# Kernel optimization log

Hardware: AMD Instinct MI355X
Metric: run time of the kernel (lower is better)

## Reference

```python
import jax, jax.numpy as jnp
import numpy as np

B, T, D, N = 32, 2048, 512, 512


def setup_inputs() -> dict:
    key = jax.random.key(0)
    ks = jax.random.split(key, 16)
    s_in = 1.0 / np.sqrt(D)
    s_h = 1.0 / np.sqrt(N)
    inp = {
        "x": jax.random.normal(ks[0], (B, T, D), dtype=jnp.float32),
        "W_i": jax.random.normal(ks[1], (D, N), dtype=jnp.float32) * s_in,
        "U_i": jax.random.normal(ks[2], (N, N), dtype=jnp.float32) * s_h,
        "W_f": jax.random.normal(ks[3], (D, N), dtype=jnp.float32) * s_in,
        "U_f": jax.random.normal(ks[4], (N, N), dtype=jnp.float32) * s_h,
        "W_g": jax.random.normal(ks[5], (D, N), dtype=jnp.float32) * s_in,
        "U_g": jax.random.normal(ks[6], (N, N), dtype=jnp.float32) * s_h,
        "W_c": jax.random.normal(ks[7], (D, N), dtype=jnp.float32) * s_in,
        "U_c": jax.random.normal(ks[8], (N, N), dtype=jnp.float32) * s_h,
        "W_o": jax.random.normal(ks[9], (N, N), dtype=jnp.float32) * s_h,
        "b_i": jnp.zeros((N,), dtype=jnp.float32),
        "b_f": jnp.zeros((N,), dtype=jnp.float32),
        "b_g": jnp.zeros((N,), dtype=jnp.float32),
        "b_c": jnp.zeros((N,), dtype=jnp.float32),
        "b_o": jnp.zeros((N,), dtype=jnp.float32),
    }
    return inp


def _lstm_forward(x, W_i, U_i, W_f, U_f, W_g, U_g, W_c, U_c, W_o,
                  b_i, b_f, b_g, b_c, b_o):
    # Precompute input-to-gate projections for all timesteps (same math,
    # hoisted out of the recurrence): [T, B, N] each
    xt = jnp.swapaxes(x, 0, 1)  # [T, B, N? no, D] -> [T, B, D]
    xi = jnp.einsum('tbd,dn->tbn', xt, W_i) + b_i
    xf = jnp.einsum('tbd,dn->tbn', xt, W_f) + b_f
    xg = jnp.einsum('tbd,dn->tbn', xt, W_g) + b_g
    xc = jnp.einsum('tbd,dn->tbn', xt, W_c) + b_c

    h0 = jnp.zeros((x.shape[0], U_i.shape[0]), dtype=x.dtype)
    c0 = jnp.zeros_like(h0)

    def step(carry, gates_t):
        h, c = carry
        xi_t, xf_t, xg_t, xc_t = gates_t
        i = jax.nn.sigmoid(xi_t + h @ U_i)
        f = jax.nn.sigmoid(xf_t + h @ U_f)
        g = jax.nn.sigmoid(xg_t + h @ U_g)  # original applies nonlin_i to g
        c_tilda = jnp.tanh(xc_t + h @ U_c)
        c_new = f * c + i * c_tilda
        h_new = g * jnp.tanh(c_new)
        return (h_new, c_new), h_new

    _, hs = jax.lax.scan(step, (h0, c0), (xi, xf, xg, xc))  # hs: [T, B, N]
    # output_fn: relu(h @ W_o + b_o), applied per timestep
    out = jax.nn.relu(jnp.einsum('tbn,nm->tbm', hs, W_o) + b_o)
    return jnp.swapaxes(out, 0, 1)  # [B, T, N]


def reference(x, W_i, U_i, W_f, U_f, W_g, U_g, W_c, U_c, W_o,
              b_i, b_f, b_g, b_c, b_o):
    return _lstm_forward(x, W_i, U_i, W_f, U_f, W_g, U_g, W_c, U_c, W_o,
                         b_i, b_f, b_g, b_c, b_o)
```

## Files before the change

### kernel.cpp

```cpp
#include <hip/hip_runtime.h>
#include <stdint.h>

#define B_ 32
#define T_ 2048
#define D_ 512
#define N_ 512
#define NG 2048

typedef _Float16 f16;
typedef _Float16 half2v __attribute__((ext_vector_type(2)));
typedef _Float16 half8  __attribute__((ext_vector_type(8)));
typedef float    float4v __attribute__((ext_vector_type(4)));
typedef unsigned long long u64;

union U32H2 { unsigned u; half2v h; };
union U4H8  { uint4 u; half8 h; };
union H16U  { f16 h; unsigned short s; };

static __device__ __forceinline__ float fast_sigmoid(float x) {
    return __builtin_amdgcn_rcpf(1.f + __expf(-x));
}
static __device__ __forceinline__ float fast_tanh(float x) {
    return 1.f - 2.f * __builtin_amdgcn_rcpf(1.f + __expf(2.f * x));
}

__global__ void prep_cast(const float* __restrict__ x, f16* __restrict__ x16) {
    long i = ((long)blockIdx.x * 256 + threadIdx.x) * 4;
    float4 v = *(const float4*)(x + i);
    union { f16 h[4]; uint2 u; } pk;
    pk.h[0] = (f16)v.x; pk.h[1] = (f16)v.y; pk.h[2] = (f16)v.z; pk.h[3] = (f16)v.w;
    *(uint2*)(x16 + i) = pk.u;
}

__global__ void prep_w(const float* __restrict__ Wi, const float* __restrict__ Ui,
                       const float* __restrict__ Wf, const float* __restrict__ Uf,
                       const float* __restrict__ Wg, const float* __restrict__ Ug,
                       const float* __restrict__ Wc, const float* __restrict__ Uc,
                       const float* __restrict__ Wo,
                       const float* __restrict__ bi, const float* __restrict__ bff,
                       const float* __restrict__ bg, const float* __restrict__ bc,
                       f16* __restrict__ wt, f16* __restrict__ ut,
                       f16* __restrict__ wot, float* __restrict__ bias)
{
    const int y = blockIdx.y;
    const int e = blockIdx.x * 256 + threadIdx.x;
    if (y < 4) {
        const float* src = (y == 0) ? Wi : (y == 1) ? Wf : (y == 2) ? Wg : Wc;
        int col = e >> 9, d = e & 511;
        wt[(long)y * 512 * 512 + e] = (f16)src[(long)d * 512 + col];
    } else if (y < 8) {
        const float* src = (y == 4) ? Ui : (y == 5) ? Uf : (y == 6) ? Ug : Uc;
        int col = e >> 9, d = e & 511;
        ut[(long)(y - 4) * 512 * 512 + e] = (f16)src[(long)d * 512 + col];
    } else if (y == 8) {
        int col = e >> 9, d = e & 511;
        wot[e] = (f16)Wo[(long)d * 512 + col];
    } else {
        if (e < 2048) {
            const float* bsrc = (e < 512) ? bi : (e < 1024) ? bff : (e < 1536) ? bg : bc;
            bias[e] = bsrc[e & 511];
        }
    }
}

__launch_bounds__(256)
__global__ void gemm_xw(const f16* __restrict__ A, const f16* __restrict__ Bt,
                        const float* __restrict__ bias, f16* __restrict__ C)
{
    __shared__ f16 sA[128 * 32];
    __shared__ f16 sB[128 * 32];
    const int tid = threadIdx.x;
    const int m0 = blockIdx.y * 128;
    const int n0 = blockIdx.x * 128;
    const int wave = tid >> 6, lane = tid & 63;
    const int wm = wave >> 1, wn = wave & 1;
    const int lrow = lane & 15, quad = lane >> 4;

    float4v acc[4][4];
#pragma unroll
    for (int i = 0; i < 4; i++)
#pragma unroll
        for (int j = 0; j < 4; j++) acc[i][j] = (float4v){0.f, 0.f, 0.f, 0.f};

    const int srow = tid >> 2;
    const int sk8 = (tid & 3) * 8;

    for (int k0 = 0; k0 < 512; k0 += 32) {
#pragma unroll
        for (int rr = 0; rr < 128; rr += 64) {
            const int row = rr + srow;
            *(uint4*)&sA[row * 32 + sk8] = *(const uint4*)&A[(long)(m0 + row) * 512 + k0 + sk8];
            *(uint4*)&sB[row * 32 + sk8] = *(const uint4*)&Bt[(long)(n0 + row) * 512 + k0 + sk8];
        }
        __syncthreads();
        half8 af[4], bf[4];
#pragma unroll
        for (int mi = 0; mi < 4; mi++)
            af[mi] = *(half8*)&sA[(wm * 64 + mi * 16 + lrow) * 32 + quad * 8];
#pragma unroll
        for (int ni = 0; ni < 4; ni++)
            bf[ni] = *(half8*)&sB[(wn * 64 + ni * 16 + lrow) * 32 + quad * 8];
#pragma unroll
        for (int mi = 0; mi < 4; mi++)
#pragma unroll
            for (int ni = 0; ni < 4; ni++)
                acc[mi][ni] = __builtin_amdgcn_mfma_f32_16x16x32_f16(af[mi], bf[ni], acc[mi][ni], 0, 0, 0);
        __syncthreads();
    }
#pragma unroll
    for (int mi = 0; mi < 4; mi++)
#pragma unroll
        for (int ni = 0; ni < 4; ni++)
#pragma unroll
            for (int r = 0; r < 4; r++) {
                int m = m0 + wm * 64 + mi * 16 + quad * 4 + r;
                int n = n0 + wn * 64 + ni * 16 + lrow;
                C[(long)m * NG + n] = (f16)(acc[mi][ni][r] + bias[n]);
            }
}

__launch_bounds__(256)
__global__ void gemm_hw(const f16* __restrict__ A, const f16* __restrict__ Bt,
                        const float* __restrict__ bias, float* __restrict__ out)
{
    __shared__ f16 sA[128 * 32];
    __shared__ f16 sB[128 * 32];
    const int tid = threadIdx.x;
    const int m0 = blockIdx.y * 128;
    const int n0 = blockIdx.x * 128;
    const int wave = tid >> 6, lane = tid & 63;
    const int wm = wave >> 1, wn = wave & 1;
    const int lrow = lane & 15, quad = lane >> 4;

    float4v acc[4][4];
#pragma unroll
    for (int i = 0; i < 4; i++)
#pragma unroll
        for (int j = 0; j < 4; j++) acc[i][j] = (float4v){0.f, 0.f, 0.f, 0.f};

    const int srow = tid >> 2;
    const int sk8 = (tid & 3) * 8;

    for (int k0 = 0; k0 < 512; k0 += 32) {
#pragma unroll
        for (int rr = 0; rr < 128; rr += 64) {
            const int row = rr + srow;
            *(uint4*)&sA[row * 32 + sk8] = *(const uint4*)&A[(long)(m0 + row) * 512 + k0 + sk8];
            *(uint4*)&sB[row * 32 + sk8] = *(const uint4*)&Bt[(long)(n0 + row) * 512 + k0 + sk8];
        }
        __syncthreads();
        half8 af[4], bf[4];
#pragma unroll
        for (int mi = 0; mi < 4; mi++)
            af[mi] = *(half8*)&sA[(wm * 64 + mi * 16 + lrow) * 32 + quad * 8];
#pragma unroll
        for (int ni = 0; ni < 4; ni++)
            bf[ni] = *(half8*)&sB[(wn * 64 + ni * 16 + lrow) * 32 + quad * 8];
#pragma unroll
        for (int mi = 0; mi < 4; mi++)
#pragma unroll
            for (int ni = 0; ni < 4; ni++)
                acc[mi][ni] = __builtin_amdgcn_mfma_f32_16x16x32_f16(af[mi], bf[ni], acc[mi][ni], 0, 0, 0);
        __syncthreads();
    }
#pragma unroll
    for (int mi = 0; mi < 4; mi++)
#pragma unroll
        for (int ni = 0; ni < 4; ni++)
#pragma unroll
            for (int r = 0; r < 4; r++) {
                int m = m0 + wm * 64 + mi * 16 + quad * 4 + r;
                int n = n0 + wn * 64 + ni * 16 + lrow;
                float v = acc[mi][ni][r] + bias[n];
                v = fmaxf(v, 0.f);
                int t = m >> 5, b = m & 31;
                out[(long)b * (T_ * (long)N_) + (long)t * N_ + n] = v;
            }
}

__launch_bounds__(512, 2)
__global__ void lstm_rec(const f16* __restrict__ Ut,
                         const f16* __restrict__ xpre,
                         u64* __restrict__ hg64,
                         unsigned* __restrict__ hs32,
                         int unused)
{
    const int tid = threadIdx.x;
    const int bb = blockIdx.x & 31;
    const int s  = blockIdx.x >> 5;
    const int w    = tid >> 6;
    const int lane = tid & 63;
    const int quad = lane >> 4;
    const int lcol = lane & 15;
    const int g0    = w >> 1;
    const int ebase = (w & 1) * 32;

    __shared__ __align__(16) unsigned hbuf32[256];
    __shared__ float prelds[256];

    half8 bf0[16], bf1[16];
    {
        const int e0 = ebase + lcol;
        const int e1 = ebase + 16 + lcol;
        const f16* bp0 = Ut + (long)(g0 * 512 + s * 64 + e0) * 512 + quad * 8;
        const f16* bp1 = Ut + (long)(g0 * 512 + s * 64 + e1) * 512 + quad * 8;
#pragma unroll
        for (int ks = 0; ks < 16; ks++) {
            bf0[ks] = *(const half8*)(bp0 + ks * 32);
            bf1[ks] = *(const half8*)(bp1 + ks * 32);
        }
    }

    if (tid < 256) hbuf32[tid] = 0u;
    float cst = 0.f;
    __syncthreads();

    const f16* xb = xpre + (long)bb * T_ * NG + s * 64 + tid;

    f16 xc_i = (f16)0, xc_f = (f16)0, xc_g = (f16)0, xc_c = (f16)0;
    if (tid < 64) {
        xc_i = xb[0]; xc_f = xb[512]; xc_g = xb[1024]; xc_c = xb[1536];
    }

    for (int t = 0; t < T_; ++t) {
        if (t > 0 && tid < 256) {
            const u64* slot = hg64 + (size_t)(t & 1) * 8192 + bb * 256 + tid;
            const unsigned tag = (unsigned)t;
            u64 v;
            while ((unsigned)((v = __hip_atomic_load(slot, __ATOMIC_RELAXED,
                                                     __HIP_MEMORY_SCOPE_AGENT)) >> 32) != tag)
                __builtin_amdgcn_s_sleep(1);
            hbuf32[tid] = (unsigned)v;
        }
        asm volatile("" ::: "memory");
        __builtin_amdgcn_sched_barrier(0);

        f16 xn_i = (f16)0, xn_f = (f16)0, xn_g = (f16)0, xn_c = (f16)0;
        if (t < T_ - 1 && tid < 64) {
            const f16* p = xb + (long)(t + 1) * NG;
            xn_i = p[0]; xn_f = p[512]; xn_g = p[1024]; xn_c = p[1536];
        }

        asm volatile("s_waitcnt lgkmcnt(0)" ::: "memory");
        __builtin_amdgcn_s_barrier();
        __builtin_amdgcn_sched_barrier(0);

        float4v a0 = {0.f, 0.f, 0.f, 0.f}, a1 = {0.f, 0.f, 0.f, 0.f};
        float4v a2 = {0.f, 0.f, 0.f, 0.f}, a3 = {0.f, 0.f, 0.f, 0.f};
#pragma unroll
        for (int ks = 0; ks < 16; ks += 2) {
            U4H8 av0, av1;
            av0.u = *(const uint4*)&hbuf32[ks * 16 + quad * 4];
            av1.u = *(const uint4*)&hbuf32[(ks + 1) * 16 + quad * 4];
            a0 = __builtin_amdgcn_mfma_f32_16x16x32_f16(av0.h, bf0[ks],     a0, 0, 0, 0);
            a1 = __builtin_amdgcn_mfma_f32_16x16x32_f16(av0.h, bf1[ks],     a1, 0, 0, 0);
            a2 = __builtin_amdgcn_mfma_f32_16x16x32_f16(av1.h, bf0[ks + 1], a2, 0, 0, 0);
            a3 = __builtin_amdgcn_mfma_f32_16x16x32_f16(av1.h, bf1[ks + 1], a3, 0, 0, 0);
        }
        if (lane < 32)
            prelds[w * 32 + lane] = (lane < 16) ? (a0[0] + a2[0]) : (a1[0] + a3[0]);

        asm volatile("s_waitcnt lgkmcnt(0)" ::: "memory");
        __builtin_amdgcn_s_barrier();
        __builtin_amdgcn_sched_barrier(0);

        if (tid < 64) {
            float pre_i = prelds[tid]       + (float)xc_i;
            float pre_f = prelds[64 + tid]  + (float)xc_f;
            float pre_g = prelds[128 + tid] + (float)xc_g;
            float pre_c = prelds[192 + tid] + (float)xc_c;
            float gi = fast_sigmoid(pre_i);
            float gf = fast_sigmoid(pre_f);
            float gg = fast_sigmoid(pre_g);
            float ct = fast_tanh(pre_c);
            cst = gf * cst + gi * ct;
            float h = gg * fast_tanh(cst);

            H16U cv; cv.h = (f16)h;
            unsigned hx = (unsigned)cv.s;
            unsigned lo = __shfl(hx, 2 * lane);
            unsigned hi = __shfl(hx, 2 * lane + 1);
            if (lane < 32) {
                unsigned pk = lo | (hi << 16);
                u64 pv = ((u64)(unsigned)(t + 1) << 32) | (u64)pk;
                __hip_atomic_store(hg64 + (size_t)((t + 1) & 1) * 8192 + bb * 256 + s * 32 + lane,
                                   pv, __ATOMIC_RELAXED, __HIP_MEMORY_SCOPE_AGENT);
                hs32[((long)t * B_ + bb) * 256 + s * 32 + lane] = pk;
            }
        }
        xc_i = xn_i; xc_f = xn_f; xc_g = xn_g; xc_c = xn_c;
    }
}

extern "C" void kernel_launch(void* const* d_in, const int* in_sizes, int n_in,
                              void* d_out, int out_size, void* d_ws, size_t ws_size,
                              hipStream_t stream)
{
    const float* x  = (const float*)d_in[0];
    const float* Wi = (const float*)d_in[1];
    const float* Ui = (const float*)d_in[2];
    const float* Wf = (const float*)d_in[3];
    const float* Uf = (const float*)d_in[4];
    const float* Wg = (const float*)d_in[5];
    const float* Ug = (const float*)d_in[6];
    const float* Wc = (const float*)d_in[7];
    const float* Uc = (const float*)d_in[8];
    const float* Wo = (const float*)d_in[9];
    const float* bi = (const float*)d_in[10];
    const float* bf = (const float*)d_in[11];
    const float* bg = (const float*)d_in[12];
    const float* bc = (const float*)d_in[13];
    const float* bo = (const float*)d_in[14];

    char* ws = (char*)d_ws;
    f16*      x16   = (f16*)(ws + 0L);
    f16*      xpre  = (f16*)(ws + 67108864L);
    f16*      hs    = (f16*)(ws + 335544320L);
    f16*      wt    = (f16*)(ws + 402653184L);
    f16*      ut    = (f16*)(ws + 404750336L);
    f16*      wot   = (f16*)(ws + 406847488L);
    float*    bias  = (float*)(ws + 407371776L);
    u64*      hg64  = (u64*)(ws + 407379968L);

    prep_cast<<<dim3(32768), dim3(256), 0, stream>>>(x, x16);
    prep_w<<<dim3(1024, 10), dim3(256), 0, stream>>>(Wi, Ui, Wf, Uf, Wg, Ug, Wc, Uc, Wo,
                                                     bi, bf, bg, bc, wt, ut, wot, bias);
    gemm_xw<<<dim3(16, 512), dim3(256), 0, stream>>>(x16, wt, bias, xpre);
    lstm_rec<<<dim3(256), dim3(512), 0, stream>>>(ut, xpre, hg64, (unsigned*)hs, 0);
    gemm_hw<<<dim3(4, 512), dim3(256), 0, stream>>>(hs, wot, bo, (float*)d_out);
}
```

Before: 3.704 ms.

## Repartition recurrence blocks to process two batch rows per block with narrower hidden slices

The recurrent kernel now gives each block a pair of batch rows and a 32-wide hidden slice, where before it had one batch row and a 64-wide slice. Each wave keeps one set of U fragments instead of two, which halves register use for the weights. The MFMA A-operand rows now carry two batch rows' hidden states, so one MFMA does more useful work. Each block must now poll and gather 512 h entries per step instead of 256, and the grid launch must match the new mapping (16 row-pairs x 16 slices).

```diff
diff --git a/kernel.cpp b/kernel.cpp
--- a/kernel.cpp
+++ b/kernel.cpp
@@ -185,52 +185,53 @@
                          unsigned* __restrict__ hs32,
                          int unused)
 {
+    const int bid = blockIdx.x;
+    const int r = bid & 15;
+    const int s = bid >> 4;
     const int tid = threadIdx.x;
-    const int bb = blockIdx.x & 31;
-    const int s  = blockIdx.x >> 5;
     const int w    = tid >> 6;
     const int lane = tid & 63;
     const int quad = lane >> 4;
     const int lcol = lane & 15;
-    const int g0    = w >> 1;
-    const int ebase = (w & 1) * 32;
-
-    __shared__ __align__(16) unsigned hbuf32[256];
+    const int g0   = w >> 1;
+    const int half = w & 1;
+
+    __shared__ __align__(16) unsigned hbuf[512];
     __shared__ float prelds[256];
 
-    half8 bf0[16], bf1[16];
+    half8 bfr[16];
     {
-        const int e0 = ebase + lcol;
-        const int e1 = ebase + 16 + lcol;
-        const f16* bp0 = Ut + (long)(g0 * 512 + s * 64 + e0) * 512 + quad * 8;
-        const f16* bp1 = Ut + (long)(g0 * 512 + s * 64 + e1) * 512 + quad * 8;
-#pragma unroll
-        for (int ks = 0; ks < 16; ks++) {
-            bf0[ks] = *(const half8*)(bp0 + ks * 32);
-            bf1[ks] = *(const half8*)(bp1 + ks * 32);
-        }
-    }
-
-    if (tid < 256) hbuf32[tid] = 0u;
+        const f16* bp = Ut + (long)(g0 * 512 + s * 32 + half * 16 + lcol) * 512 + quad * 8;
+#pragma unroll
+        for (int ks = 0; ks < 16; ks++)
+            bfr[ks] = *(const half8*)(bp + ks * 32);
+    }
+
+    hbuf[tid] = 0u;
     float cst = 0.f;
     __syncthreads();
 
-    const f16* xb = xpre + (long)bb * T_ * NG + s * 64 + tid;
+    const int gbatch = tid >> 5;
+    const int ge = tid & 31;
+    const long bglob = 2L * r + gbatch;
+    const f16* xb = xpre + bglob * T_ * NG + s * 32 + ge;
 
     f16 xc_i = (f16)0, xc_f = (f16)0, xc_g = (f16)0, xc_c = (f16)0;
     if (tid < 64) {
         xc_i = xb[0]; xc_f = xb[512]; xc_g = xb[1024]; xc_c = xb[1536];
     }
 
+    const unsigned aoff = (unsigned)((lcol >> 3) * 256 + quad * 4);
+
     for (int t = 0; t < T_; ++t) {
-        if (t > 0 && tid < 256) {
-            const u64* slot = hg64 + (size_t)(t & 1) * 8192 + bb * 256 + tid;
+        if (t > 0) {
+            const u64* slot = hg64 + (size_t)(t & 1) * 8192 + (size_t)r * 512 + tid;
             const unsigned tag = (unsigned)t;
             u64 v;
             while ((unsigned)((v = __hip_atomic_load(slot, __ATOMIC_RELAXED,
                                                      __HIP_MEMORY_SCOPE_AGENT)) >> 32) != tag)
                 __builtin_amdgcn_s_sleep(1);
-            hbuf32[tid] = (unsigned)v;
+            hbuf[tid] = (unsigned)v;
         }
         asm volatile("" ::: "memory");
         __builtin_amdgcn_sched_barrier(0);
@@ -245,30 +246,33 @@
         __builtin_amdgcn_s_barrier();
         __builtin_amdgcn_sched_barrier(0);
 
-        float4v a0 = {0.f, 0.f, 0.f, 0.f}, a1 = {0.f, 0.f, 0.f, 0.f};
-        float4v a2 = {0.f, 0.f, 0.f, 0.f}, a3 = {0.f, 0.f, 0.f, 0.f};
-#pragma unroll
-        for (int ks = 0; ks < 16; ks += 2) {
-            U4H8 av0, av1;
-            av0.u = *(const uint4*)&hbuf32[ks * 16 + quad * 4];
-            av1.u = *(const uint4*)&hbuf32[(ks + 1) * 16 + quad * 4];
-            a0 = __builtin_amdgcn_mfma_f32_16x16x32_f16(av0.h, bf0[ks],     a0, 0, 0, 0);
-            a1 = __builtin_amdgcn_mfma_f32_16x16x32_f16(av0.h, bf1[ks],     a1, 0, 0, 0);
-            a2 = __builtin_amdgcn_mfma_f32_16x16x32_f16(av1.h, bf0[ks + 1], a2, 0, 0, 0);
-            a3 = __builtin_amdgcn_mfma_f32_16x16x32_f16(av1.h, bf1[ks + 1], a3, 0, 0, 0);
-        }
-        if (lane < 32)
-            prelds[w * 32 + lane] = (lane < 16) ? (a0[0] + a2[0]) : (a1[0] + a3[0]);
+        float4v ac0 = {0.f,0.f,0.f,0.f}, ac1 = {0.f,0.f,0.f,0.f};
+        float4v ac2 = {0.f,0.f,0.f,0.f}, ac3 = {0.f,0.f,0.f,0.f};
+#pragma unroll
+        for (int ks = 0; ks < 16; ks += 4) {
+            U4H8 a0, a1, a2, a3;
+            a0.u = *(const uint4*)&hbuf[aoff + (ks + 0) * 16];
+            a1.u = *(const uint4*)&hbuf[aoff + (ks + 1) * 16];
+            a2.u = *(const uint4*)&hbuf[aoff + (ks + 2) * 16];
+            a3.u = *(const uint4*)&hbuf[aoff + (ks + 3) * 16];
+            ac0 = __builtin_amdgcn_mfma_f32_16x16x32_f16(a0.h, bfr[ks + 0], ac0, 0, 0, 0);
+            ac1 = __builtin_amdgcn_mfma_f32_16x16x32_f16(a1.h, bfr[ks + 1], ac1, 0, 0, 0);
+            ac2 = __builtin_amdgcn_mfma_f32_16x16x32_f16(a2.h, bfr[ks + 2], ac2, 0, 0, 0);
+            ac3 = __builtin_amdgcn_mfma_f32_16x16x32_f16(a3.h, bfr[ks + 3], ac3, 0, 0, 0);
+        }
+        if ((quad & 1) == 0)
+            prelds[(quad >> 1) * 128 + g0 * 32 + half * 16 + lcol] =
+                (ac0[0] + ac1[0]) + (ac2[0] + ac3[0]);
 
         asm volatile("s_waitcnt lgkmcnt(0)" ::: "memory");
         __builtin_amdgcn_s_barrier();
         __builtin_amdgcn_sched_barrier(0);
 
         if (tid < 64) {
-            float pre_i = prelds[tid]       + (float)xc_i;
-            float pre_f = prelds[64 + tid]  + (float)xc_f;
-            float pre_g = prelds[128 + tid] + (float)xc_g;
-            float pre_c = prelds[192 + tid] + (float)xc_c;
+            float pre_i = prelds[gbatch * 128 +       ge] + (float)xc_i;
+            float pre_f = prelds[gbatch * 128 +  32 + ge] + (float)xc_f;
+            float pre_g = prelds[gbatch * 128 +  64 + ge] + (float)xc_g;
+            float pre_c = prelds[gbatch * 128 +  96 + ge] + (float)xc_c;
             float gi = fast_sigmoid(pre_i);
             float gf = fast_sigmoid(pre_f);
             float gg = fast_sigmoid(pre_g);
@@ -278,14 +282,18 @@
 
             H16U cv; cv.h = (f16)h;
             unsigned hx = (unsigned)cv.s;
-            unsigned lo = __shfl(hx, 2 * lane);
-            unsigned hi = __shfl(hx, 2 * lane + 1);
-            if (lane < 32) {
+            const int base = lane & 32;
+            const int j = lane & 15;
+            unsigned lo = __shfl(hx, base + 2 * j);
+            unsigned hi = __shfl(hx, base + 2 * j + 1);
+            if ((lane & 31) < 16) {
+                const int pb = lane >> 5;
                 unsigned pk = lo | (hi << 16);
                 u64 pv = ((u64)(unsigned)(t + 1) << 32) | (u64)pk;
-                __hip_atomic_store(hg64 + (size_t)((t + 1) & 1) * 8192 + bb * 256 + s * 32 + lane,
+                __hip_atomic_store(hg64 + (size_t)((t + 1) & 1) * 8192 + (size_t)r * 512
+                                        + (size_t)pb * 256 + s * 16 + j,
                                    pv, __ATOMIC_RELAXED, __HIP_MEMORY_SCOPE_AGENT);
-                hs32[((long)t * B_ + bb) * 256 + s * 32 + lane] = pk;
+                hs32[((long)t * B_ + (2 * r + pb)) * 256 + s * 16 + j] = pk;
             }
         }
         xc_i = xn_i; xc_f = xn_f; xc_g = xn_g; xc_c = xn_c;
```

After: 4.051 ms. +9.4%, slower.

## Remap recurrent MFMA columns so each wave computes complete gate sets locally

Applied to the files above, without the earlier changes.

Reassigns the recurrent weight columns so each wave's 16 MFMA output columns hold all four gates (i,f,g,c) for a few hidden units. The gates are then exchanged with lane shuffles instead of going through shared memory, which removes the second block barrier per timestep and spreads the nonlinearity across all waves. The change also double-buffers the LDS h buffer and drops the sleep in the spin-wait, which cuts per-step latency on the serial recurrence at the cost of more polling traffic and more shuffle and select work.

```diff
diff --git a/kernel.cpp b/kernel.cpp
--- a/kernel.cpp
+++ b/kernel.cpp
@@ -192,35 +192,26 @@
     const int lane = tid & 63;
     const int quad = lane >> 4;
     const int lcol = lane & 15;
-    const int g0    = w >> 1;
-    const int ebase = (w & 1) * 32;
-
-    __shared__ __align__(16) unsigned hbuf32[256];
-    __shared__ float prelds[256];
-
-    half8 bf0[16], bf1[16];
-    {
-        const int e0 = ebase + lcol;
-        const int e1 = ebase + 16 + lcol;
-        const f16* bp0 = Ut + (long)(g0 * 512 + s * 64 + e0) * 512 + quad * 8;
-        const f16* bp1 = Ut + (long)(g0 * 512 + s * 64 + e1) * 512 + quad * 8;
-#pragma unroll
-        for (int ks = 0; ks < 16; ks++) {
-            bf0[ks] = *(const half8*)(bp0 + ks * 32);
-            bf1[ks] = *(const half8*)(bp1 + ks * 32);
-        }
-    }
-
-    if (tid < 256) hbuf32[tid] = 0u;
-    float cst = 0.f;
+    const int g  = lcol >> 2;
+    const int eo = lcol & 3;
+
+    __shared__ __align__(16) unsigned hbuf[2][256];
+
+    half8 bfr[2][16];
+#pragma unroll
+    for (int tau = 0; tau < 2; tau++) {
+        const f16* bp = Ut + (long)(g * 512 + s * 64 + 8 * w + tau * 4 + eo) * 512 + quad * 8;
+#pragma unroll
+        for (int ks = 0; ks < 16; ks++)
+            bfr[tau][ks] = *(const half8*)(bp + ks * 32);
+    }
+
+    if (tid < 256) hbuf[0][tid] = 0u;
+    float cst0 = 0.f, cst1 = 0.f;
     __syncthreads();
 
-    const f16* xb = xpre + (long)bb * T_ * NG + s * 64 + tid;
-
-    f16 xc_i = (f16)0, xc_f = (f16)0, xc_g = (f16)0, xc_c = (f16)0;
-    if (tid < 64) {
-        xc_i = xb[0]; xc_f = xb[512]; xc_g = xb[1024]; xc_c = xb[1536];
-    }
+    const f16* xb = xpre + (long)bb * T_ * NG + (g * 512 + s * 64 + 8 * w + eo);
+    f16 xc0 = xb[0], xc1 = xb[4];
 
     for (int t = 0; t < T_; ++t) {
         if (t > 0 && tid < 256) {
@@ -228,67 +219,78 @@
             const unsigned tag = (unsigned)t;
             u64 v;
             while ((unsigned)((v = __hip_atomic_load(slot, __ATOMIC_RELAXED,
-                                                     __HIP_MEMORY_SCOPE_AGENT)) >> 32) != tag)
-                __builtin_amdgcn_s_sleep(1);
-            hbuf32[tid] = (unsigned)v;
+                                                     __HIP_MEMORY_SCOPE_AGENT)) >> 32) != tag) {}
+            hbuf[t & 1][tid] = (unsigned)v;
         }
         asm volatile("" ::: "memory");
         __builtin_amdgcn_sched_barrier(0);
 
-        f16 xn_i = (f16)0, xn_f = (f16)0, xn_g = (f16)0, xn_c = (f16)0;
-        if (t < T_ - 1 && tid < 64) {
+        f16 xn0 = (f16)0, xn1 = (f16)0;
+        if (t < T_ - 1) {
             const f16* p = xb + (long)(t + 1) * NG;
-            xn_i = p[0]; xn_f = p[512]; xn_g = p[1024]; xn_c = p[1536];
+            xn0 = p[0]; xn1 = p[4];
         }
 
         asm volatile("s_waitcnt lgkmcnt(0)" ::: "memory");
         __builtin_amdgcn_s_barrier();
         __builtin_amdgcn_sched_barrier(0);
 
-        float4v a0 = {0.f, 0.f, 0.f, 0.f}, a1 = {0.f, 0.f, 0.f, 0.f};
-        float4v a2 = {0.f, 0.f, 0.f, 0.f}, a3 = {0.f, 0.f, 0.f, 0.f};
+        const unsigned* hb = hbuf[t & 1];
+        float4v a00 = {0.f,0.f,0.f,0.f}, a01 = {0.f,0.f,0.f,0.f};
+        float4v a10 = {0.f,0.f,0.f,0.f}, a11 = {0.f,0.f,0.f,0.f};
 #pragma unroll
         for (int ks = 0; ks < 16; ks += 2) {
             U4H8 av0, av1;
-            av0.u = *(const uint4*)&hbuf32[ks * 16 + quad * 4];
-            av1.u = *(const uint4*)&hbuf32[(ks + 1) * 16 + quad * 4];
-            a0 = __builtin_amdgcn_mfma_f32_16x16x32_f16(av0.h, bf0[ks],     a0, 0, 0, 0);
-            a1 = __builtin_amdgcn_mfma_f32_16x16x32_f16(av0.h, bf1[ks],     a1, 0, 0, 0);
-            a2 = __builtin_amdgcn_mfma_f32_16x16x32_f16(av1.h, bf0[ks + 1], a2, 0, 0, 0);
-            a3 = __builtin_amdgcn_mfma_f32_16x16x32_f16(av1.h, bf1[ks + 1], a3, 0, 0, 0);
-        }
-        if (lane < 32)
-            prelds[w * 32 + lane] = (lane < 16) ? (a0[0] + a2[0]) : (a1[0] + a3[0]);
-
-        asm volatile("s_waitcnt lgkmcnt(0)" ::: "memory");
-        __builtin_amdgcn_s_barrier();
-        __builtin_amdgcn_sched_barrier(0);
-
-        if (tid < 64) {
-            float pre_i = prelds[tid]       + (float)xc_i;
-            float pre_f = prelds[64 + tid]  + (float)xc_f;
-            float pre_g = prelds[128 + tid] + (float)xc_g;
-            float pre_c = prelds[192 + tid] + (float)xc_c;
-            float gi = fast_sigmoid(pre_i);
-            float gf = fast_sigmoid(pre_f);
-            float gg = fast_sigmoid(pre_g);
-            float ct = fast_tanh(pre_c);
-            cst = gf * cst + gi * ct;
-            float h = gg * fast_tanh(cst);
-
-            H16U cv; cv.h = (f16)h;
-            unsigned hx = (unsigned)cv.s;
-            unsigned lo = __shfl(hx, 2 * lane);
-            unsigned hi = __shfl(hx, 2 * lane + 1);
-            if (lane < 32) {
-                unsigned pk = lo | (hi << 16);
-                u64 pv = ((u64)(unsigned)(t + 1) << 32) | (u64)pk;
-                __hip_atomic_store(hg64 + (size_t)((t + 1) & 1) * 8192 + bb * 256 + s * 32 + lane,
-                                   pv, __ATOMIC_RELAXED, __HIP_MEMORY_SCOPE_AGENT);
-                hs32[((long)t * B_ + bb) * 256 + s * 32 + lane] = pk;
-            }
-        }
-        xc_i = xn_i; xc_f = xn_f; xc_g = xn_g; xc_c = xn_c;
+            av0.u = *(const uint4*)&hb[ks * 16 + quad * 4];
+            av1.u = *(const uint4*)&hb[(ks + 1) * 16 + quad * 4];
+            a00 = __builtin_amdgcn_mfma_f32_16x16x32_f16(av0.h, bfr[0][ks],     a00, 0, 0, 0);
+            a10 = __builtin_amdgcn_mfma_f32_16x16x32_f16(av0.h, bfr[1][ks],     a10, 0, 0, 0);
+            a01 = __builtin_amdgcn_mfma_f32_16x16x32_f16(av1.h, bfr[0][ks + 1], a01, 0, 0, 0);
+            a11 = __builtin_amdgcn_mfma_f32_16x16x32_f16(av1.h, bfr[1][ks + 1], a11, 0, 0, 0);
+        }
+        float pre0 = (a00[0] + a01[0]) + (float)xc0;
+        float pre1 = (a10[0] + a11[0]) + (float)xc1;
+
+        const float mm = (g == 3) ? 2.f : -1.f;
+        float e0 = __expf(mm * pre0), e1 = __expf(mm * pre1);
+        float r0 = __builtin_amdgcn_rcpf(1.f + e0), r1 = __builtin_amdgcn_rcpf(1.f + e1);
+        float act0 = (g == 3) ? 1.f - 2.f * r0 : r0;
+        float act1 = (g == 3) ? 1.f - 2.f * r1 : r1;
+        float p1_0 = __shfl_xor(act0, 4),  p2_0 = __shfl_xor(act0, 8),  p3_0 = __shfl_xor(p1_0, 8);
+        float p1_1 = __shfl_xor(act1, 4),  p2_1 = __shfl_xor(act1, 8),  p3_1 = __shfl_xor(p1_1, 8);
+        float gi0 = (g == 0) ? act0 : (g == 1) ? p1_0 : (g == 2) ? p2_0 : p3_0;
+        float gf0 = (g == 1) ? act0 : (g == 0) ? p1_0 : (g == 3) ? p2_0 : p3_0;
+        float gg0 = (g == 2) ? act0 : (g == 3) ? p1_0 : (g == 0) ? p2_0 : p3_0;
+        float ct0 = (g == 3) ? act0 : (g == 2) ? p1_0 : (g == 1) ? p2_0 : p3_0;
+        float gi1 = (g == 0) ? act1 : (g == 1) ? p1_1 : (g == 2) ? p2_1 : p3_1;
+        float gf1 = (g == 1) ? act1 : (g == 0) ? p1_1 : (g == 3) ? p2_1 : p3_1;
+        float gg1 = (g == 2) ? act1 : (g == 3) ? p1_1 : (g == 0) ? p2_1 : p3_1;
+        float ct1 = (g == 3) ? act1 : (g == 2) ? p1_1 : (g == 1) ? p2_1 : p3_1;
+
+        cst0 = gf0 * cst0 + gi0 * ct0;
+        cst1 = gf1 * cst1 + gi1 * ct1;
+        float h0 = gg0 * fast_tanh(cst0);
+        float h1 = gg1 * fast_tanh(cst1);
+
+        H16U c0v, c1v; c0v.h = (f16)h0; c1v.h = (f16)h1;
+        unsigned hx0 = (unsigned)c0v.s, hx1 = (unsigned)c1v.s;
+        unsigned hi0 = __shfl(hx0, lane + 1);
+        unsigned hi1 = __shfl(hx1, lane + 1);
+        if (lane == 0 || lane == 2) {
+            const int k = lane >> 1;
+            unsigned pk0 = hx0 | (hi0 << 16);
+            unsigned pk1 = hx1 | (hi1 << 16);
+            const size_t base = (size_t)((t + 1) & 1) * 8192 + (size_t)bb * 256 + s * 32 + 4 * w;
+            const u64 tagw = (u64)(unsigned)(t + 1) << 32;
+            __hip_atomic_store(hg64 + base + k,     tagw | (u64)pk0,
+                               __ATOMIC_RELAXED, __HIP_MEMORY_SCOPE_AGENT);
+            __hip_atomic_store(hg64 + base + 2 + k, tagw | (u64)pk1,
+                               __ATOMIC_RELAXED, __HIP_MEMORY_SCOPE_AGENT);
+            const long hbase = ((long)t * B_ + bb) * 256 + s * 32 + 4 * w;
+            hs32[hbase + k]     = pk0;
+            hs32[hbase + 2 + k] = pk1;
+        }
+        xc0 = xn0; xc1 = xn1;
     }
 }
 
```

After: 4.949 ms. 33.6% more time.
